# Kernel optimization log

Measured on AMD Instinct MI355X. Metric: run time of the kernel, lower is better.

The kernel has to match this reference:

```python
import jax, jax.numpy as jnp
import numpy as np

N_HEAD = 4
HEAD_DIM = 32
D_MODEL = 128
NEG_BIG = -1.0e9  # note: source uses (mask-1)*(-1e9), reproduced faithfully
LN_EPS = 1e-05


def _layer_norm(x, gain, bias):
    mean = jnp.mean(x, axis=-1, keepdims=True)
    var = jnp.mean(jnp.square(x - mean), axis=-1, keepdims=True)
    return gain * (x - mean) / jnp.sqrt(var + LN_EPS) + bias


def setup_inputs() -> dict:
    key = jax.random.key(0)
    ks = jax.random.split(key, 6)
    L, S, D = 8, 2048, D_MODEL
    x = jax.random.normal(ks[0], (L, S, D), dtype=jnp.float32)
    mask = jnp.ones((L, S), dtype=jnp.int32)
    qkv_w = jax.random.normal(ks[1], (D, 3 * D), dtype=jnp.float32) * (1.0 / np.sqrt(D))
    out_w = jax.random.normal(ks[2], (D, D), dtype=jnp.float32) * (1.0 / np.sqrt(D))
    w1 = jax.random.normal(ks[3], (D, 384), dtype=jnp.float32) * (1.0 / np.sqrt(D))
    b1 = jnp.zeros((384,), dtype=jnp.float32)
    w2 = jax.random.normal(ks[4], (384, D), dtype=jnp.float32) * (1.0 / np.sqrt(384))
    b2 = jnp.zeros((D,), dtype=jnp.float32)
    g1 = jnp.ones((D,), dtype=jnp.float32)
    be1 = jnp.zeros((D,), dtype=jnp.float32)
    g2 = jnp.ones((D,), dtype=jnp.float32)
    be2 = jnp.zeros((D,), dtype=jnp.float32)
    return {"x": x, "mask": mask, "qkv_w": qkv_w, "out_w": out_w,
            "w1": w1, "b1": b1, "w2": w2, "b2": b2,
            "g1": g1, "be1": be1, "g2": g2, "be2": be2}


def reference(x, mask, qkv_w, out_w, w1, b1, w2, b2, g1, be1, g2, be2):
    # x: [L, S, D] -- the python list axis of the original module is L (each element batch=1)
    L, S, D = x.shape
    H, hd = N_HEAD, HEAD_DIM
    m = mask.astype(jnp.float32)  # [L, S]

    # QKV projection (single shared weight, split into q/k/v)
    qkv = jnp.einsum('lsd,de->lse', x, qkv_w)  # [L, S, 3D]
    q, k, v = jnp.split(qkv, 3, axis=-1)
    q = q.reshape(L, S, H, hd).transpose(0, 2, 1, 3)  # [L, H, S, hd]
    k = k.reshape(L, S, H, hd).transpose(0, 2, 1, 3)
    v = v.reshape(L, S, H, hd).transpose(0, 2, 1, 3)

    scale = 1.0 / np.sqrt(D // H)
    scores = jnp.einsum('lhqd,lhkd->lhqk', q, k) * scale  # [L, H, S, S]

    # outer-product padding mask, faithful to source: amask*scores + (amask-1)*(-1e9)
    amask = (m[:, None, :, None] * m[:, None, None, :])  # [L, 1, S, S]
    masked = amask * scores + (amask - 1.0) * NEG_BIG
    attn = jax.nn.softmax(masked, axis=-1)

    ctx = jnp.einsum('lhqk,lhkd->lhqd', attn, v)  # [L, H, S, hd]
    ctx = ctx.transpose(0, 2, 1, 3).reshape(L, S, D)
    attn_out = jnp.einsum('lsd,de->lse', ctx, out_w)  # output projection

    # residual + LN1 (dropout rate 0.0 -> identity)
    h = _layer_norm(attn_out + x, g1, be1)

    # FFN: Dense(384, relu) -> Dense(128, relu)
    ff = jax.nn.relu(jnp.einsum('lsd,df->lsf', h, w1) + b1)
    ff = jax.nn.relu(jnp.einsum('lsf,fd->lsd', ff, w2) + b2)

    # residual + LN2
    out = _layer_norm(ff + h, g2, be2)
    return out
```

## Files before the change

### kernel.cpp

```cpp
#include <hip/hip_runtime.h>
#include <hip/hip_bf16.h>

typedef __attribute__((ext_vector_type(8))) short bf16x8;
typedef __attribute__((ext_vector_type(4))) float f32x4;
typedef unsigned short u16;
typedef unsigned int u32;

__device__ __forceinline__ u32 bfr(float x) {
  u32 u = __float_as_uint(x);
  return (u + 0x7fffu + ((u >> 16) & 1u)) >> 16;
}
__device__ __forceinline__ u32 pk2(float lo, float hi) {
  return bfr(lo) | (bfr(hi) << 16);
}
__device__ __forceinline__ u32 cvtpk(float lo, float hi) {
  u32 r;
  asm("v_cvt_pk_bf16_f32 %0, %1, %2" : "=v"(r) : "v"(lo), "v"(hi));
  return r;
}

__device__ __forceinline__ f32x4 mfma16(bf16x8 a, bf16x8 b, f32x4 c) {
  return __builtin_amdgcn_mfma_f32_16x16x32_bf16(a, b, c, 0, 0, 0);
}

__global__ __launch_bounds__(256) void prep_all(
    const float* __restrict__ qkv_w, const float* __restrict__ out_w,
    const float* __restrict__ w1, const float* __restrict__ w2,
    const int* __restrict__ mask,
    u16* __restrict__ qkvT, u16* __restrict__ outT,
    u16* __restrict__ w1T, u16* __restrict__ w2T, int* __restrict__ flag) {
  __shared__ int wbad[4];
  int b = blockIdx.x;
  if (b >= 640) {
    int l = b - 640;
    int bad = 0;
    for (int i = threadIdx.x; i < 2048; i += 256)
      bad |= (mask[l * 2048 + i] != 1);
    unsigned long long bl = __ballot(bad != 0);
    if ((threadIdx.x & 63) == 0) wbad[threadIdx.x >> 6] = (bl != 0ULL) ? 1 : 0;
    __syncthreads();
    if (threadIdx.x == 0)
      flag[l] = (wbad[0] | wbad[1] | wbad[2] | wbad[3]) ? 0 : 1;
    return;
  }
  int idx = b * 256 + threadIdx.x;
  if (idx < 49152) {
    int n = idx >> 7, k = idx & 127;
    qkvT[idx] = (u16)bfr(qkv_w[k * 384 + n]);
  } else if (idx < 49152 + 16384) {
    int i = idx - 49152;
    int n = i >> 7, k = i & 127;
    outT[i] = (u16)bfr(out_w[k * 128 + n]);
  } else if (idx < 49152 + 16384 + 49152) {
    int i = idx - 49152 - 16384;
    int n = i >> 7, k = i & 127;
    w1T[i] = (u16)bfr(w1[k * 384 + n]);
  } else if (idx < 163840) {
    int i = idx - 49152 - 16384 - 49152;
    int n = i / 384, k = i - n * 384;
    w2T[i] = (u16)bfr(w2[k * 128 + n]);
  }
}

template <int K, int N, int EPI, bool CONVA>
__global__ __launch_bounds__(256) void gemm_bf16(
    const void* __restrict__ Av, const u16* __restrict__ WT,
    const float* __restrict__ bias,
    u16* __restrict__ O0, u16* __restrict__ O1, u16* __restrict__ O2) {
  __shared__ u16 lds_a[64 * 136];
  __shared__ u16 lds_b[64 * 136];
  const int m0 = blockIdx.x * 64, n0 = blockIdx.y * 64;
  const int tid = threadIdx.x, lane = tid & 63, wv = tid >> 6;
  const int wm = wv >> 1, wn = wv & 1, c = lane & 15, g = lane >> 4;

  f32x4 acc[2][2] = {};
  for (int kt = 0; kt < K / 128; ++kt) {
    if (kt) __syncthreads();
    for (int i = tid; i < 1024; i += 256) {
      int row = i >> 4, cc = (i & 15) * 8;
      if constexpr (CONVA) {
        const float* Af = (const float*)Av;
        const float4* pa =
            (const float4*)(Af + (size_t)(m0 + row) * K + kt * 128 + cc);
        float4 v0 = pa[0], v1 = pa[1];
        uint4 aw = {pk2(v0.x, v0.y), pk2(v0.z, v0.w), pk2(v1.x, v1.y),
                    pk2(v1.z, v1.w)};
        *(uint4*)(&lds_a[row * 136 + cc]) = aw;
      } else {
        const u16* Au = (const u16*)Av;
        *(uint4*)(&lds_a[row * 136 + cc]) =
            *(const uint4*)(Au + (size_t)(m0 + row) * K + kt * 128 + cc);
      }
      *(uint4*)(&lds_b[row * 136 + cc]) =
          *(const uint4*)(WT + (size_t)(n0 + row) * K + kt * 128 + cc);
    }
    __syncthreads();
#pragma unroll
    for (int ks = 0; ks < 4; ++ks) {
      bf16x8 a0 = *(bf16x8*)(&lds_a[(wm * 32 + c) * 136 + ks * 32 + 8 * g]);
      bf16x8 a1 = *(bf16x8*)(&lds_a[(wm * 32 + 16 + c) * 136 + ks * 32 + 8 * g]);
      bf16x8 b0 = *(bf16x8*)(&lds_b[(wn * 32 + c) * 136 + ks * 32 + 8 * g]);
      bf16x8 b1 = *(bf16x8*)(&lds_b[(wn * 32 + 16 + c) * 136 + ks * 32 + 8 * g]);
      acc[0][0] = mfma16(a0, b0, acc[0][0]);
      acc[0][1] = mfma16(a0, b1, acc[0][1]);
      acc[1][0] = mfma16(a1, b0, acc[1][0]);
      acc[1][1] = mfma16(a1, b1, acc[1][1]);
    }
  }
#pragma unroll
  for (int mi = 0; mi < 2; ++mi)
#pragma unroll
    for (int ni = 0; ni < 2; ++ni) {
      const int n = n0 + wn * 32 + ni * 16 + c;
      const int mb = m0 + wm * 32 + mi * 16 + 4 * g;
      if constexpr (EPI == 2) {
        float bv = bias[n];
#pragma unroll
        for (int r = 0; r < 4; ++r)
          O0[(size_t)(mb + r) * N + n] =
              (u16)bfr(fmaxf(acc[mi][ni][r] + bv, 0.f));
      } else {
        const int reg = n >> 7, hh = (n >> 5) & 3, d = n & 31;
        const int l = mb >> 11, s = mb & 2047;
        const size_t lh = (size_t)l * 4 + hh;
        if (reg == 0) {
#pragma unroll
          for (int r = 0; r < 4; ++r)
            O0[(lh * 2048 + s + r) * 32 + d] =
                (u16)bfr(acc[mi][ni][r] * 0.17677669529663687f);
        } else if (reg == 1) {
#pragma unroll
          for (int r = 0; r < 4; ++r)
            O1[(lh * 2048 + s + r) * 32 + d] = (u16)bfr(acc[mi][ni][r]);
        } else {
          uint2 w = {pk2(acc[mi][ni][0], acc[mi][ni][1]),
                     pk2(acc[mi][ni][2], acc[mi][ni][3])};
          *(uint2*)(O2 + (lh * 32 + d) * 2048 + s) = w;
        }
      }
    }
}

template <int K, bool RELU>
__global__ __launch_bounds__(256) void gemm_ln(
    const u16* __restrict__ A, const u16* __restrict__ WT,
    const float* __restrict__ bias, const float* __restrict__ resid,
    const float* __restrict__ gain, const float* __restrict__ lnb,
    float* __restrict__ outf, u16* __restrict__ outb) {
  __shared__ u16 lds_a[64 * 136];
  __shared__ u16 lds_b[128 * 136];
  const int m0 = blockIdx.x * 64;
  const int tid = threadIdx.x, lane = tid & 63, wv = tid >> 6;
  const int c = lane & 15, g = lane >> 4;

  f32x4 acc[8] = {};
  for (int kt = 0; kt < K / 128; ++kt) {
    if (kt) __syncthreads();
    for (int i = tid; i < 1024; i += 256) {
      int row = i >> 4, cc = (i & 15) * 8;
      *(uint4*)(&lds_a[row * 136 + cc]) =
          *(const uint4*)(A + (size_t)(m0 + row) * K + kt * 128 + cc);
    }
    for (int i = tid; i < 2048; i += 256) {
      int row = i >> 4, cc = (i & 15) * 8;
      *(uint4*)(&lds_b[row * 136 + cc]) =
          *(const uint4*)(WT + (size_t)row * K + kt * 128 + cc);
    }
    __syncthreads();
#pragma unroll
    for (int ks = 0; ks < 4; ++ks) {
      bf16x8 a = *(bf16x8*)(&lds_a[(wv * 16 + c) * 136 + ks * 32 + 8 * g]);
#pragma unroll
      for (int ni = 0; ni < 8; ++ni) {
        bf16x8 b = *(bf16x8*)(&lds_b[(ni * 16 + c) * 136 + ks * 32 + 8 * g]);
        acc[ni] = mfma16(a, b, acc[ni]);
      }
    }
  }
  const int rbase = m0 + wv * 16 + 4 * g;
  float gv[8], lb[8], bv[8];
#pragma unroll
  for (int ni = 0; ni < 8; ++ni) {
    gv[ni] = gain[ni * 16 + c];
    lb[ni] = lnb[ni * 16 + c];
    if constexpr (RELU) bv[ni] = bias[ni * 16 + c];
  }
  float t[8][4];
  float sum[4] = {0.f, 0.f, 0.f, 0.f}, sq[4] = {0.f, 0.f, 0.f, 0.f};
#pragma unroll
  for (int ni = 0; ni < 8; ++ni) {
#pragma unroll
    for (int r = 0; r < 4; ++r) {
      float v = acc[ni][r];
      if constexpr (RELU) v = fmaxf(v + bv[ni], 0.f);
      v += resid[(size_t)(rbase + r) * 128 + ni * 16 + c];
      t[ni][r] = v;
      sum[r] += v;
      sq[r] += v * v;
    }
  }
#pragma unroll
  for (int off = 1; off < 16; off <<= 1) {
#pragma unroll
    for (int r = 0; r < 4; ++r) {
      sum[r] += __shfl_xor(sum[r], off);
      sq[r] += __shfl_xor(sq[r], off);
    }
  }
#pragma unroll
  for (int r = 0; r < 4; ++r) {
    float mean = sum[r] * (1.0f / 128.0f);
    float var = sq[r] * (1.0f / 128.0f) - mean * mean;
    float inv = rsqrtf(var + 1e-5f);
#pragma unroll
    for (int ni = 0; ni < 8; ++ni) {
      float o = gv[ni] * (t[ni][r] - mean) * inv + lb[ni];
      outf[(size_t)(rbase + r) * 128 + ni * 16 + c] = o;
      if (outb) outb[(size_t)(rbase + r) * 128 + ni * 16 + c] = (u16)bfr(o);
    }
  }
}

__global__ __launch_bounds__(256) void attn4(
    const u16* __restrict__ Qs, const u16* __restrict__ Kb,
    const u16* __restrict__ Vt, const int* __restrict__ mask,
    const int* __restrict__ mflag, u16* __restrict__ ctx) {
  __shared__ u16 lds_k[2][64 * 40];
  __shared__ u16 lds_vt[2][32 * 72];
  __shared__ u16 lds_p[4][16 * 72];
  __shared__ float lds_mk[2][64];

  const int bid = blockIdx.x;
  const int qt = bid & 31, lh = bid >> 5;
  const int tid = threadIdx.x, lane = tid & 63, wv = tid >> 6;
  const int c = lane & 15, g = lane >> 4;
  const int tok0 = (lh >> 2) * 2048;
  const int h = lh & 3;
  const int allone = mflag[lh >> 2];

  const int qrow = qt * 64 + wv * 16 + c;
  const bf16x8 qf = *(const bf16x8*)(Qs + ((size_t)lh * 2048 + qrow) * 32 + 8 * g);
  const float mq = allone ? 1.0f : (float)mask[tok0 + qrow];

  const int kr_ = tid & 63, kc_ = tid >> 6;
  const int vr_ = tid >> 3, vc_ = tid & 7;
  const u16* kbase = Kb + ((size_t)lh * 2048) * 32 + kr_ * 32 + kc_ * 8;
  const u16* vbase = Vt + ((size_t)lh * 32 + vr_) * 2048 + vc_ * 8;

  uint4 krg, vrg;
  float mkv = 0.f;
  auto issue = [&](int kt0) {
    krg = *(const uint4*)(kbase + (size_t)kt0 * 32);
    vrg = *(const uint4*)(vbase + kt0);
    if (!allone && tid < 64) mkv = (float)mask[tok0 + kt0 + tid];
  };
  auto commit = [&](int buf) {
    *(uint4*)(&lds_k[buf][kr_ * 40 + kc_ * 8]) = krg;
    *(uint4*)(&lds_vt[buf][vr_ * 72 + vc_ * 8]) = vrg;
    if (!allone && tid < 64) lds_mk[buf][tid] = mkv;
  };

  issue(0);
  commit(0);
  __syncthreads();

  f32x4 acc0 = {0.f, 0.f, 0.f, 0.f}, acc1 = {0.f, 0.f, 0.f, 0.f};
  float m_run = -1e30f, lsum = 0.f;
  const f32x4 zf = {0.f, 0.f, 0.f, 0.f};

  for (int t = 0; t < 32; ++t) {
    const int cur = t & 1;
    if (t < 31) issue((t + 1) * 64);

    f32x4 s[4];
#pragma unroll
    for (int j = 0; j < 4; ++j) {
      bf16x8 a = *(bf16x8*)(&lds_k[cur][(16 * j + c) * 40 + 8 * g]);
      s[j] = mfma16(a, qf, zf);
    }
    float sv[16];
    if (allone) {
#pragma unroll
      for (int j = 0; j < 4; ++j)
#pragma unroll
        for (int r = 0; r < 4; ++r) sv[4 * j + r] = s[j][r];
    } else {
#pragma unroll
      for (int j = 0; j < 4; ++j) {
        float4 mk4 = *(float4*)(&lds_mk[cur][16 * j + 4 * g]);
        const float* mkp = (const float*)&mk4;
#pragma unroll
        for (int r = 0; r < 4; ++r) {
          float am = mq * mkp[r];
          sv[4 * j + r] = am * s[j][r] + (am - 1.0f) * (-1e9f);
        }
      }
    }
    float tmax = sv[0];
#pragma unroll
    for (int i = 1; i < 16; ++i) tmax = fmaxf(tmax, sv[i]);
    tmax = fmaxf(tmax, __shfl_xor(tmax, 16));
    tmax = fmaxf(tmax, __shfl_xor(tmax, 32));
    if (!__all(tmax <= m_run + 8.0f)) {
      float mnew = fmaxf(m_run, tmax);
      float corr = __expf(m_run - mnew);
      m_run = mnew;
      lsum *= corr;
      acc0 *= corr;
      acc1 *= corr;
    }
    float p[16], psum = 0.f;
#pragma unroll
    for (int i = 0; i < 16; ++i) {
      p[i] = __expf(sv[i] - m_run);
      psum += p[i];
    }
    lsum += psum;
#pragma unroll
    for (int j = 0; j < 4; ++j) {
      uint2 w = {cvtpk(p[4 * j], p[4 * j + 1]), cvtpk(p[4 * j + 2], p[4 * j + 3])};
      *(uint2*)(&lds_p[wv][c * 72 + 16 * j + 4 * g]) = w;
    }
    bf16x8 pb0 = *(bf16x8*)(&lds_p[wv][c * 72 + 8 * g]);
    bf16x8 pb1 = *(bf16x8*)(&lds_p[wv][c * 72 + 32 + 8 * g]);
    bf16x8 v00 = *(bf16x8*)(&lds_vt[cur][c * 72 + 8 * g]);
    bf16x8 v01 = *(bf16x8*)(&lds_vt[cur][c * 72 + 32 + 8 * g]);
    bf16x8 v10 = *(bf16x8*)(&lds_vt[cur][(16 + c) * 72 + 8 * g]);
    bf16x8 v11 = *(bf16x8*)(&lds_vt[cur][(16 + c) * 72 + 32 + 8 * g]);
    acc0 = mfma16(v00, pb0, acc0);
    acc0 = mfma16(v01, pb1, acc0);
    acc1 = mfma16(v10, pb0, acc1);
    acc1 = mfma16(v11, pb1, acc1);

    if (t < 31) commit(cur ^ 1);
    __syncthreads();
  }
  float lt = lsum;
  lt += __shfl_xor(lt, 16);
  lt += __shfl_xor(lt, 32);
  float inv = 1.0f / lt;
  u16* op = ctx + (size_t)(tok0 + qrow) * 128 + h * 32;
  uint2 o0 = {cvtpk(acc0[0] * inv, acc0[1] * inv),
              cvtpk(acc0[2] * inv, acc0[3] * inv)};
  uint2 o1 = {cvtpk(acc1[0] * inv, acc1[1] * inv),
              cvtpk(acc1[2] * inv, acc1[3] * inv)};
  *(uint2*)(op + 4 * g) = o0;
  *(uint2*)(op + 16 + 4 * g) = o1;
}

extern "C" void kernel_launch(void* const* d_in, const int* in_sizes, int n_in,
                              void* d_out, int out_size, void* d_ws,
                              size_t ws_size, hipStream_t stream) {
  (void)in_sizes; (void)n_in; (void)out_size; (void)ws_size;
  const float* x = (const float*)d_in[0];
  const int* mask = (const int*)d_in[1];
  const float* qkv_w = (const float*)d_in[2];
  const float* out_w = (const float*)d_in[3];
  const float* w1 = (const float*)d_in[4];
  const float* b1 = (const float*)d_in[5];
  const float* w2 = (const float*)d_in[6];
  const float* b2 = (const float*)d_in[7];
  const float* g1 = (const float*)d_in[8];
  const float* be1 = (const float*)d_in[9];
  const float* g2 = (const float*)d_in[10];
  const float* be2 = (const float*)d_in[11];
  float* out = (float*)d_out;

  char* ws = (char*)d_ws;
  const size_t MB = 1 << 20;
  u16* Qs = (u16*)(ws);
  u16* Kb = (u16*)(ws + 4 * MB);
  u16* Vt = (u16*)(ws + 8 * MB);
  u16* ff_bf = (u16*)(ws);
  u16* ctx_bf = (u16*)(ws + 12 * MB);
  float* h = (float*)(ws + 16 * MB);
  u16* h_bf = (u16*)(ws + 24 * MB);
  u16* qkvT = (u16*)(ws + 32 * MB);
  u16* outT = qkvT + 384 * 128;
  u16* w1T = outT + 128 * 128;
  u16* w2T = w1T + 384 * 128;
  int* mflag = (int*)(ws + 33 * MB);

  prep_all<<<648, 256, 0, stream>>>(qkv_w, out_w, w1, w2, mask, qkvT, outT,
                                    w1T, w2T, mflag);
  gemm_bf16<128, 384, 3, true><<<dim3(256, 6), 256, 0, stream>>>(
      (const void*)x, qkvT, nullptr, Qs, Kb, Vt);
  attn4<<<1024, 256, 0, stream>>>(Qs, Kb, Vt, mask, mflag, ctx_bf);
  gemm_ln<128, false><<<256, 256, 0, stream>>>(
      ctx_bf, outT, nullptr, x, g1, be1, h, h_bf);
  gemm_bf16<128, 384, 2, false><<<dim3(256, 6), 256, 0, stream>>>(
      (const void*)h_bf, w1T, b1, ff_bf, nullptr, nullptr);
  gemm_ln<384, true><<<256, 256, 0, stream>>>(
      ff_bf, w2T, b2, h, g2, be2, out, nullptr);
}
```

Baseline: 97.46 us.

## Widen GEMM tiles to 64x128 and compute softmax row sums with MFMA

The QKV and FFN1 GEMMs now use 64x128 output tiles, with each wave owning 16 rows by 128 columns. This halves the grid and the number of times the A tile is loaded and converted, but uses more LDS and registers per block. In attention, the per-thread exp-sum and cross-lane shuffles are replaced by an extra MFMA against a ones matrix, which puts the row sum into an accumulator. That sum is taken from the bf16-rounded probabilities, so it now matches the values used in P·V.

```diff
diff --git a/kernel.cpp b/kernel.cpp
--- a/kernel.cpp
+++ b/kernel.cpp
@@ -63,17 +63,17 @@
 }
 
 template <int K, int N, int EPI, bool CONVA>
-__global__ __launch_bounds__(256) void gemm_bf16(
+__global__ __launch_bounds__(256) void gemm_bf16w(
     const void* __restrict__ Av, const u16* __restrict__ WT,
     const float* __restrict__ bias,
     u16* __restrict__ O0, u16* __restrict__ O1, u16* __restrict__ O2) {
   __shared__ u16 lds_a[64 * 136];
-  __shared__ u16 lds_b[64 * 136];
-  const int m0 = blockIdx.x * 64, n0 = blockIdx.y * 64;
+  __shared__ u16 lds_b[128 * 136];
+  const int m0 = blockIdx.x * 64, n0 = blockIdx.y * 128;
   const int tid = threadIdx.x, lane = tid & 63, wv = tid >> 6;
-  const int wm = wv >> 1, wn = wv & 1, c = lane & 15, g = lane >> 4;
-
-  f32x4 acc[2][2] = {};
+  const int c = lane & 15, g = lane >> 4;
+
+  f32x4 acc[8] = {};
   for (int kt = 0; kt < K / 128; ++kt) {
     if (kt) __syncthreads();
     for (int i = tid; i < 1024; i += 256) {
@@ -91,54 +91,52 @@
         *(uint4*)(&lds_a[row * 136 + cc]) =
             *(const uint4*)(Au + (size_t)(m0 + row) * K + kt * 128 + cc);
       }
+    }
+    for (int i = tid; i < 2048; i += 256) {
+      int row = i >> 4, cc = (i & 15) * 8;
       *(uint4*)(&lds_b[row * 136 + cc]) =
           *(const uint4*)(WT + (size_t)(n0 + row) * K + kt * 128 + cc);
     }
     __syncthreads();
 #pragma unroll
     for (int ks = 0; ks < 4; ++ks) {
-      bf16x8 a0 = *(bf16x8*)(&lds_a[(wm * 32 + c) * 136 + ks * 32 + 8 * g]);
-      bf16x8 a1 = *(bf16x8*)(&lds_a[(wm * 32 + 16 + c) * 136 + ks * 32 + 8 * g]);
-      bf16x8 b0 = *(bf16x8*)(&lds_b[(wn * 32 + c) * 136 + ks * 32 + 8 * g]);
-      bf16x8 b1 = *(bf16x8*)(&lds_b[(wn * 32 + 16 + c) * 136 + ks * 32 + 8 * g]);
-      acc[0][0] = mfma16(a0, b0, acc[0][0]);
-      acc[0][1] = mfma16(a0, b1, acc[0][1]);
-      acc[1][0] = mfma16(a1, b0, acc[1][0]);
-      acc[1][1] = mfma16(a1, b1, acc[1][1]);
-    }
-  }
-#pragma unroll
-  for (int mi = 0; mi < 2; ++mi)
-#pragma unroll
-    for (int ni = 0; ni < 2; ++ni) {
-      const int n = n0 + wn * 32 + ni * 16 + c;
-      const int mb = m0 + wm * 32 + mi * 16 + 4 * g;
-      if constexpr (EPI == 2) {
-        float bv = bias[n];
+      bf16x8 a = *(bf16x8*)(&lds_a[(wv * 16 + c) * 136 + ks * 32 + 8 * g]);
+#pragma unroll
+      for (int ni = 0; ni < 8; ++ni) {
+        bf16x8 b = *(bf16x8*)(&lds_b[(ni * 16 + c) * 136 + ks * 32 + 8 * g]);
+        acc[ni] = mfma16(a, b, acc[ni]);
+      }
+    }
+  }
+  const int rbase = m0 + wv * 16 + 4 * g;
+#pragma unroll
+  for (int ni = 0; ni < 8; ++ni) {
+    const int n = n0 + ni * 16 + c;
+    if constexpr (EPI == 2) {
+      float bv = bias[n];
+#pragma unroll
+      for (int r = 0; r < 4; ++r)
+        O0[(size_t)(rbase + r) * N + n] =
+            (u16)bfr(fmaxf(acc[ni][r] + bv, 0.f));
+    } else {
+      const int reg = n >> 7, hh = (n >> 5) & 3, d = n & 31;
+      const int l = rbase >> 11, s = rbase & 2047;
+      const size_t lh = (size_t)l * 4 + hh;
+      if (reg == 0) {
 #pragma unroll
         for (int r = 0; r < 4; ++r)
-          O0[(size_t)(mb + r) * N + n] =
-              (u16)bfr(fmaxf(acc[mi][ni][r] + bv, 0.f));
+          O0[(lh * 2048 + s + r) * 32 + d] =
+              (u16)bfr(acc[ni][r] * 0.17677669529663687f);
+      } else if (reg == 1) {
+#pragma unroll
+        for (int r = 0; r < 4; ++r)
+          O1[(lh * 2048 + s + r) * 32 + d] = (u16)bfr(acc[ni][r]);
       } else {
-        const int reg = n >> 7, hh = (n >> 5) & 3, d = n & 31;
-        const int l = mb >> 11, s = mb & 2047;
-        const size_t lh = (size_t)l * 4 + hh;
-        if (reg == 0) {
-#pragma unroll
-          for (int r = 0; r < 4; ++r)
-            O0[(lh * 2048 + s + r) * 32 + d] =
-                (u16)bfr(acc[mi][ni][r] * 0.17677669529663687f);
-        } else if (reg == 1) {
-#pragma unroll
-          for (int r = 0; r < 4; ++r)
-            O1[(lh * 2048 + s + r) * 32 + d] = (u16)bfr(acc[mi][ni][r]);
-        } else {
-          uint2 w = {pk2(acc[mi][ni][0], acc[mi][ni][1]),
-                     pk2(acc[mi][ni][2], acc[mi][ni][3])};
-          *(uint2*)(O2 + (lh * 32 + d) * 2048 + s) = w;
-        }
-      }
-    }
+        uint2 w = {pk2(acc[ni][0], acc[ni][1]), pk2(acc[ni][2], acc[ni][3])};
+        *(uint2*)(O2 + (lh * 32 + d) * 2048 + s) = w;
+      }
+    }
+  }
 }
 
 template <int K, bool RELU>
@@ -265,8 +263,12 @@
   __syncthreads();
 
   f32x4 acc0 = {0.f, 0.f, 0.f, 0.f}, acc1 = {0.f, 0.f, 0.f, 0.f};
-  float m_run = -1e30f, lsum = 0.f;
+  f32x4 accL = {0.f, 0.f, 0.f, 0.f};
+  float m_run = -1e30f;
   const f32x4 zf = {0.f, 0.f, 0.f, 0.f};
+  union { u32 u[4]; bf16x8 v; } onesU;
+  onesU.u[0] = onesU.u[1] = onesU.u[2] = onesU.u[3] = 0x3F803F80u;
+  const bf16x8 onesA = onesU.v;
 
   for (int t = 0; t < 32; ++t) {
     const int cur = t & 1;
@@ -305,17 +307,13 @@
       float mnew = fmaxf(m_run, tmax);
       float corr = __expf(m_run - mnew);
       m_run = mnew;
-      lsum *= corr;
+      accL *= corr;
       acc0 *= corr;
       acc1 *= corr;
     }
-    float p[16], psum = 0.f;
-#pragma unroll
-    for (int i = 0; i < 16; ++i) {
-      p[i] = __expf(sv[i] - m_run);
-      psum += p[i];
-    }
-    lsum += psum;
+    float p[16];
+#pragma unroll
+    for (int i = 0; i < 16; ++i) p[i] = __expf(sv[i] - m_run);
 #pragma unroll
     for (int j = 0; j < 4; ++j) {
       uint2 w = {cvtpk(p[4 * j], p[4 * j + 1]), cvtpk(p[4 * j + 2], p[4 * j + 3])};
@@ -331,14 +329,13 @@
     acc0 = mfma16(v01, pb1, acc0);
     acc1 = mfma16(v10, pb0, acc1);
     acc1 = mfma16(v11, pb1, acc1);
+    accL = mfma16(onesA, pb0, accL);
+    accL = mfma16(onesA, pb1, accL);
 
     if (t < 31) commit(cur ^ 1);
     __syncthreads();
   }
-  float lt = lsum;
-  lt += __shfl_xor(lt, 16);
-  lt += __shfl_xor(lt, 32);
-  float inv = 1.0f / lt;
+  float inv = 1.0f / accL[0];
   u16* op = ctx + (size_t)(tok0 + qrow) * 128 + h * 32;
   uint2 o0 = {cvtpk(acc0[0] * inv, acc0[1] * inv),
               cvtpk(acc0[2] * inv, acc0[3] * inv)};
@@ -383,12 +380,12 @@
 
   prep_all<<<648, 256, 0, stream>>>(qkv_w, out_w, w1, w2, mask, qkvT, outT,
                                     w1T, w2T, mflag);
-  gemm_bf16<128, 384, 3, true><<<dim3(256, 6), 256, 0, stream>>>(
+  gemm_bf16w<128, 384, 3, true><<<dim3(256, 3), 256, 0, stream>>>(
       (const void*)x, qkvT, nullptr, Qs, Kb, Vt);
   attn4<<<1024, 256, 0, stream>>>(Qs, Kb, Vt, mask, mflag, ctx_bf);
   gemm_ln<128, false><<<256, 256, 0, stream>>>(
       ctx_bf, outT, nullptr, x, g1, be1, h, h_bf);
-  gemm_bf16<128, 384, 2, false><<<dim3(256, 6), 256, 0, stream>>>(
+  gemm_bf16w<128, 384, 2, false><<<dim3(256, 3), 256, 0, stream>>>(
       (const void*)h_bf, w1T, b1, ff_bf, nullptr, nullptr);
   gemm_ln<384, true><<<256, 256, 0, stream>>>(
       ff_bf, w2T, b2, h, g2, be2, out, nullptr);
```

New measurement: 106.9 us. +9.7%, slower.

## Split attention KV range into two partitions and merge with a combine kernel

Applied to the files above, without the earlier changes.

The attention kernel now processes half of the key/value sequence per block, with a second grid dimension selecting the half. This doubles the number of blocks so more of the GPU is occupied at once. Each block writes unnormalized fp32 partial outputs plus its running max and sum. A new combine kernel rescales the two partials, normalizes them and writes the bf16 context. The cost is an extra kernel launch and a round trip of fp32 partial results through global memory.

```diff
diff --git a/kernel.cpp b/kernel.cpp
--- a/kernel.cpp
+++ b/kernel.cpp
@@ -221,21 +221,23 @@
   }
 }
 
-__global__ __launch_bounds__(256) void attn4(
+__global__ __launch_bounds__(256) void attn4s(
     const u16* __restrict__ Qs, const u16* __restrict__ Kb,
     const u16* __restrict__ Vt, const int* __restrict__ mask,
-    const int* __restrict__ mflag, u16* __restrict__ ctx) {
+    const int* __restrict__ mflag, float* __restrict__ Opart,
+    float2* __restrict__ ml) {
   __shared__ u16 lds_k[2][64 * 40];
   __shared__ u16 lds_vt[2][32 * 72];
   __shared__ u16 lds_p[4][16 * 72];
   __shared__ float lds_mk[2][64];
 
   const int bid = blockIdx.x;
+  const int sp = blockIdx.y;
+  const int tbase = sp * 16;
   const int qt = bid & 31, lh = bid >> 5;
   const int tid = threadIdx.x, lane = tid & 63, wv = tid >> 6;
   const int c = lane & 15, g = lane >> 4;
   const int tok0 = (lh >> 2) * 2048;
-  const int h = lh & 3;
   const int allone = mflag[lh >> 2];
 
   const int qrow = qt * 64 + wv * 16 + c;
@@ -260,7 +262,7 @@
     if (!allone && tid < 64) lds_mk[buf][tid] = mkv;
   };
 
-  issue(0);
+  issue(tbase * 64);
   commit(0);
   __syncthreads();
 
@@ -268,9 +270,9 @@
   float m_run = -1e30f, lsum = 0.f;
   const f32x4 zf = {0.f, 0.f, 0.f, 0.f};
 
-  for (int t = 0; t < 32; ++t) {
+  for (int t = 0; t < 16; ++t) {
     const int cur = t & 1;
-    if (t < 31) issue((t + 1) * 64);
+    if (t < 15) issue((tbase + t + 1) * 64);
 
     f32x4 s[4];
 #pragma unroll
@@ -332,20 +334,36 @@
     acc1 = mfma16(v10, pb0, acc1);
     acc1 = mfma16(v11, pb1, acc1);
 
-    if (t < 31) commit(cur ^ 1);
+    if (t < 15) commit(cur ^ 1);
     __syncthreads();
   }
   float lt = lsum;
   lt += __shfl_xor(lt, 16);
   lt += __shfl_xor(lt, 32);
-  float inv = 1.0f / lt;
-  u16* op = ctx + (size_t)(tok0 + qrow) * 128 + h * 32;
-  uint2 o0 = {cvtpk(acc0[0] * inv, acc0[1] * inv),
-              cvtpk(acc0[2] * inv, acc0[3] * inv)};
-  uint2 o1 = {cvtpk(acc1[0] * inv, acc1[1] * inv),
-              cvtpk(acc1[2] * inv, acc1[3] * inv)};
-  *(uint2*)(op + 4 * g) = o0;
-  *(uint2*)(op + 16 + 4 * g) = o1;
+  float* op = Opart + (size_t)sp * 2097152 + ((size_t)lh * 2048 + qrow) * 32;
+  float4 o0 = {acc0[0], acc0[1], acc0[2], acc0[3]};
+  float4 o1 = {acc1[0], acc1[1], acc1[2], acc1[3]};
+  *(float4*)(op + 4 * g) = o0;
+  *(float4*)(op + 16 + 4 * g) = o1;
+  if (lane < 16) {
+    float2 v = {m_run, lt};
+    ml[(size_t)sp * 65536 + (size_t)lh * 2048 + qrow] = v;
+  }
+}
+
+__global__ __launch_bounds__(256) void attn_combine(
+    const float* __restrict__ Opart, const float2* __restrict__ ml,
+    u16* __restrict__ ctx) {
+  int idx = blockIdx.x * 256 + threadIdx.x;
+  int lhq = idx >> 5, d = idx & 31;
+  int lh = lhq >> 11, qrow = lhq & 2047;
+  float2 a = ml[lhq], b = ml[65536 + lhq];
+  float M = fmaxf(a.x, b.x);
+  float w0 = __expf(a.x - M), w1 = __expf(b.x - M);
+  float L = w0 * a.y + w1 * b.y;
+  float o = (w0 * Opart[idx] + w1 * Opart[2097152 + idx]) / L;
+  int tok = (lh >> 2) * 2048 + qrow, h = lh & 3;
+  ctx[(size_t)tok * 128 + h * 32 + d] = (u16)bfr(o);
 }
 
 extern "C" void kernel_launch(void* const* d_in, const int* in_sizes, int n_in,
@@ -373,6 +391,7 @@
   u16* Vt = (u16*)(ws + 8 * MB);
   u16* ff_bf = (u16*)(ws);
   u16* ctx_bf = (u16*)(ws + 12 * MB);
+  float* Opart = (float*)(ws + 16 * MB);
   float* h = (float*)(ws + 16 * MB);
   u16* h_bf = (u16*)(ws + 24 * MB);
   u16* qkvT = (u16*)(ws + 32 * MB);
@@ -380,12 +399,14 @@
   u16* w1T = outT + 128 * 128;
   u16* w2T = w1T + 384 * 128;
   int* mflag = (int*)(ws + 33 * MB);
+  float2* ml = (float2*)(ws + 34 * MB);
 
   prep_all<<<648, 256, 0, stream>>>(qkv_w, out_w, w1, w2, mask, qkvT, outT,
                                     w1T, w2T, mflag);
   gemm_bf16<128, 384, 3, true><<<dim3(256, 6), 256, 0, stream>>>(
       (const void*)x, qkvT, nullptr, Qs, Kb, Vt);
-  attn4<<<1024, 256, 0, stream>>>(Qs, Kb, Vt, mask, mflag, ctx_bf);
+  attn4s<<<dim3(1024, 2), 256, 0, stream>>>(Qs, Kb, Vt, mask, mflag, Opart, ml);
+  attn_combine<<<8192, 256, 0, stream>>>(Opart, ml, ctx_bf);
   gemm_ln<128, false><<<256, 256, 0, stream>>>(
       ctx_bf, outT, nullptr, x, g1, be1, h, h_bf);
   gemm_bf16<128, 384, 2, false><<<dim3(256, 6), 256, 0, stream>>>(
```

Result: slower. 106.3 us (+9.1%).
